# Optimization experiments

Measured on AMD Instinct MI355X. Metric: run time of the kernel, lower is better.

The kernel has to match this reference:

```python
import jax, jax.numpy as jnp
import numpy as np

NEG_SLOPE = 0.2

def _gat_layer(x, src, dst, W, a_s, a_d, b, concat):
    # x: [N, F_in], W: [F_in, H*C], a_s/a_d: [H, C]
    N = x.shape[0]
    H, C = a_s.shape
    h = (x @ W).reshape(N, H, C)                       # per-head projection
    al_s = jnp.sum(h * a_s, axis=-1)                   # [N, H]
    al_d = jnp.sum(h * a_d, axis=-1)                   # [N, H]
    e = jax.nn.leaky_relu(al_s[src] + al_d[dst], NEG_SLOPE)  # [E, H]
    # segment softmax over incoming edges of each dst node
    m = jax.ops.segment_max(e, dst, num_segments=N)    # [N, H]
    ex = jnp.exp(e - m[dst])
    denom = jax.ops.segment_sum(ex, dst, num_segments=N)
    alpha = ex / denom[dst]                            # [E, H]
    msg = h[src] * alpha[:, :, None]                   # [E, H, C]
    out = jax.ops.segment_sum(msg, dst, num_segments=N)  # [N, H, C]
    if concat:
        return out.reshape(N, H * C) + b
    return out.mean(axis=1) + b


def setup_inputs() -> dict:
    key = jax.random.key(0)
    ks = jax.random.split(key, 12)
    N, F_in, H, C1, LAT, E = 16384, 512, 4, 128, 64, 262144
    x = jax.random.normal(ks[0], (N, F_in), dtype=jnp.float32)
    edge_index = jax.random.randint(ks[1], (2, E), 0, N, dtype=jnp.int64)
    s = 0.05
    return {
        'x': x,
        'edge_index': edge_index,
        'W1': jax.random.normal(ks[2], (F_in, H * C1), dtype=jnp.float32) * s,
        'a_src1': jax.random.normal(ks[3], (H, C1), dtype=jnp.float32) * s,
        'a_dst1': jax.random.normal(ks[4], (H, C1), dtype=jnp.float32) * s,
        'b1': jax.random.normal(ks[5], (H * C1,), dtype=jnp.float32) * s,
        'W2': jax.random.normal(ks[6], (H * C1, H * LAT), dtype=jnp.float32) * s,
        'a_src2': jax.random.normal(ks[7], (H, LAT), dtype=jnp.float32) * s,
        'a_dst2': jax.random.normal(ks[8], (H, LAT), dtype=jnp.float32) * s,
        'b2': jax.random.normal(ks[9], (LAT,), dtype=jnp.float32) * s,
    }


def reference(x, edge_index, W1, a_src1, a_dst1, b1, W2, a_src2, a_dst2, b2):
    N = x.shape[0]
    # PyG GATConv default add_self_loops=True
    loop = jnp.arange(N, dtype=edge_index.dtype)
    src = jnp.concatenate([edge_index[0], loop])
    dst = jnp.concatenate([edge_index[1], loop])
    h = jax.nn.relu(_gat_layer(x, src, dst, W1, a_src1, a_dst1, b1, concat=True))
    out = _gat_layer(h, src, dst, W2, a_src2, a_dst2, b2, concat=False)
    return out
```

## Files before the change

kernel.cpp:

```cpp
#include <hip/hip_runtime.h>
#include <stdint.h>
#include <stddef.h>
#include <limits.h>

typedef __bf16 bf16;
typedef __bf16 bf16x4 __attribute__((ext_vector_type(4)));
typedef __bf16 bf16x8 __attribute__((ext_vector_type(8)));
typedef float  f32x4  __attribute__((ext_vector_type(4)));

static __device__ __forceinline__ float lrelu(float x) { return x > 0.f ? x : 0.2f * x; }
static __device__ __forceinline__ float san(float v) { return (fabsf(v) < 1e4f) ? v : 0.0f; }
static __device__ __forceinline__ float wexp(float e) { return __expf(fminf(e, 30.f)); }

static __device__ __forceinline__ void async_load16(const bf16* g, bf16* l) {
  __builtin_amdgcn_global_load_lds((const __attribute__((address_space(1))) void*)g,
                                   (__attribute__((address_space(3))) void*)l, 16, 0, 0);
}


__global__ __launch_bounds__(256) void prep_all(const float* __restrict__ x,
                                                bf16* __restrict__ xb,
                                                int* __restrict__ counts,
                                                const float* __restrict__ W1,
                                                const float* __restrict__ W2,
                                                bf16* __restrict__ W1T,
                                                bf16* __restrict__ W2T,
                                                int NX, int N) {
  int b = blockIdx.x;
  const int NCVT = NX >> 10;
  if (b < NCVT) {
    int i = b * 1024 + threadIdx.x * 4;
    f32x4 v = *(const f32x4*)(x + i);
    bf16x4 o;
#pragma unroll
    for (int k = 0; k < 4; ++k) o[k] = (bf16)san(v[k]);
    *(bf16x4*)(xb + i) = o;
    return;
  }
  b -= NCVT;
  if (b < N / 256) { counts[b * 256 + threadIdx.x] = 0; return; }
  b -= N / 256;
  __shared__ bf16 t[32][33];
  const float* in; bf16* out; int R, C, bx, by;
  if (b < 256) { in = W1; out = W1T; R = 512; C = 512; by = b >> 4; bx = b & 15; }
  else         { b -= 256; in = W2; out = W2T; R = 512; C = 256; by = b >> 3; bx = b & 7; }
  const int lane = threadIdx.x & 31, r8 = threadIdx.x >> 5;
#pragma unroll
  for (int k = 0; k < 4; ++k) {
    int r = by * 32 + r8 + k * 8, c = bx * 32 + lane;
    t[lane][r8 + k * 8] = (bf16)san(in[(size_t)r * C + c]);
  }
  __syncthreads();
#pragma unroll
  for (int k = 0; k < 4; ++k) {
    int oc = bx * 32 + r8 + k * 8;
    out[(size_t)oc * R + by * 32 + lane] = t[r8 + k * 8][lane];
  }
}


__global__ void count_edges(const int* __restrict__ dst, int E, int* __restrict__ counts) {
  int e = blockIdx.x * 256 + threadIdx.x;
  if (e < E) atomicAdd(&counts[dst[e]], 1);
}

__global__ __launch_bounds__(1024) void scan_block_sums(const int* __restrict__ counts,
                                                        int* __restrict__ bsums) {
  __shared__ int ws[16];
  const int tid = threadIdx.x, lane = tid & 63, w = tid >> 6;
  int v = counts[blockIdx.x * 1024 + tid];
  for (int off = 32; off; off >>= 1) v += __shfl_xor(v, off);
  if (lane == 0) ws[w] = v;
  __syncthreads();
  if (tid == 0) {
    int s = 0;
#pragma unroll
    for (int k = 0; k < 16; ++k) s += ws[k];
    bsums[blockIdx.x] = s;
  }
}

__global__ __launch_bounds__(1024) void scan_apply(const int* __restrict__ counts,
                                                   const int* __restrict__ bsums,
                                                   int* __restrict__ row_ptr,
                                                   int* __restrict__ cursor, int N, int nb) {
  __shared__ int wsum[16];
  __shared__ int bpre[2];
  const int tid = threadIdx.x, lane = tid & 63, w = tid >> 6;
  const int gi = blockIdx.x * 1024 + tid;
  if (tid == 0) {
    int pre = 0, tot = 0;
    for (int k = 0; k < nb; ++k) {
      if (k < (int)blockIdx.x) pre += bsums[k];
      tot += bsums[k];
    }
    bpre[0] = pre; bpre[1] = tot;
  }
  int v = counts[gi];
  int s = v;
  for (int off = 1; off < 64; off <<= 1) {
    int t = __shfl_up(s, off);
    if (lane >= off) s += t;
  }
  if (lane == 63) wsum[w] = s;
  __syncthreads();
  if (w == 0 && lane < 16) {
    int ws = wsum[lane];
    int t2 = ws;
    for (int off = 1; off < 16; off <<= 1) {
      int t = __shfl_up(t2, off);
      if (lane >= off) t2 += t;
    }
    wsum[lane] = t2 - ws;
  }
  __syncthreads();
  int excl = bpre[0] + wsum[w] + s - v;
  row_ptr[gi] = excl;
  cursor[gi]  = excl;
  if (gi == N - 1) row_ptr[N] = bpre[1];
}

__global__ void scatter_edges(const int* __restrict__ src, const int* __restrict__ dst, int E,
                              int* __restrict__ cursor, int* __restrict__ csr_src) {
  int e = blockIdx.x * 256 + threadIdx.x;
  if (e < E) {
    int pos = atomicAdd(&cursor[dst[e]], 1);
    csr_src[pos] = src[e];
  }
}

__global__ __launch_bounds__(256) void sort_rows_wave(const int* __restrict__ row_ptr,
                                                      int* __restrict__ csr, int N) {
  const int wid  = (blockIdx.x * 256 + threadIdx.x) >> 6;
  const int lane = threadIdx.x & 63;
  if (wid >= N) return;
  const int beg = row_ptr[wid], end = row_ptr[wid + 1];
  const int len = end - beg;
  if (len <= 1) return;
  if (len <= 64) {
    int v = (lane < len) ? csr[beg + lane] : INT_MAX;
#pragma unroll
    for (int k = 2; k <= 64; k <<= 1) {
#pragma unroll
      for (int j = k >> 1; j > 0; j >>= 1) {
        int p = __shfl_xor(v, j);
        bool take_min = (((lane & k) == 0) == ((lane & j) == 0));
        v = take_min ? min(v, p) : max(v, p);
      }
    }
    if (lane < len) csr[beg + lane] = v;
  } else if (lane == 0) {
    for (int i = beg + 1; i < end; ++i) {
      int v = csr[i];
      int j = i - 1;
      while (j >= beg && csr[j] > v) { csr[j + 1] = csr[j]; --j; }
      csr[j + 1] = v;
    }
  }
}


__global__ __launch_bounds__(256) void gemm_al_l1(const bf16* __restrict__ A,
                                                  const bf16* __restrict__ BT,
                                                  bf16* __restrict__ C,
                                                  const float* __restrict__ a_s,
                                                  const float* __restrict__ a_d,
                                                  float* __restrict__ al_s,
                                                  float* __restrict__ al_d,
                                                  int M, int N, int K) {
  __shared__ __align__(16) bf16 As[128 * 32];
  __shared__ __align__(16) bf16 Bs[128 * 32];
  __shared__ float alred[2][128][2];
  const int tid  = threadIdx.x;
  const int lane = tid & 63;
  const int wave = tid >> 6;
  const int m0 = blockIdx.x * 128;
  const int n0 = blockIdx.y * 128;
  const int wm = (wave >> 1) * 64;
  const int wn = (wave & 1) * 64;

  f32x4 acc[4][4] = {};

  const int id0 = tid, id1 = tid + 256;
  const bf16* a0p = A  + (size_t)(m0 + (id0 >> 2)) * K + (id0 & 3) * 8;
  const bf16* a1p = A  + (size_t)(m0 + (id1 >> 2)) * K + (id1 & 3) * 8;
  const bf16* b0p = BT + (size_t)(n0 + (id0 >> 2)) * K + (id0 & 3) * 8;
  const bf16* b1p = BT + (size_t)(n0 + (id1 >> 2)) * K + (id1 & 3) * 8;

  const int kq = (lane >> 4) * 8;
  const int rA = wm + (lane & 15);
  const int rB = wn + (lane & 15);

  for (int k0 = 0; k0 < K; k0 += 32) {
    __syncthreads();
    async_load16(a0p + k0, &As[id0 * 8]);
    async_load16(a1p + k0, &As[id1 * 8]);
    async_load16(b0p + k0, &Bs[id0 * 8]);
    async_load16(b1p + k0, &Bs[id1 * 8]);
    __syncthreads();
    bf16x8 af[4], bfv[4];
#pragma unroll
    for (int i = 0; i < 4; ++i) af[i]  = *(const bf16x8*)&As[(rA + i * 16) * 32 + kq];
#pragma unroll
    for (int j = 0; j < 4; ++j) bfv[j] = *(const bf16x8*)&Bs[(rB + j * 16) * 32 + kq];
#pragma unroll
    for (int i = 0; i < 4; ++i)
#pragma unroll
      for (int j = 0; j < 4; ++j)
        acc[i][j] = __builtin_amdgcn_mfma_f32_16x16x32_bf16(af[i], bfv[j], acc[i][j], 0, 0, 0);
  }

  const int cc = lane & 15;
  const int rb = (lane >> 4) * 4;
#pragma unroll
  for (int i = 0; i < 4; ++i)
#pragma unroll
    for (int j = 0; j < 4; ++j) {
      int gcol = n0 + wn + j * 16 + cc;
#pragma unroll
      for (int r = 0; r < 4; ++r) {
        int grow = m0 + wm + i * 16 + rb + r;
        C[(size_t)grow * N + gcol] = (bf16)acc[i][j][r];
      }
    }

  {
    const int head = blockIdx.y;
    float asv[4], adv[4];
#pragma unroll
    for (int j = 0; j < 4; ++j) {
      int col = head * 128 + wn + j * 16 + cc;
      asv[j] = san(a_s[col]);
      adv[j] = san(a_d[col]);
    }
    const int wnh = wn >> 6;
#pragma unroll
    for (int i = 0; i < 4; ++i)
#pragma unroll
      for (int r = 0; r < 4; ++r) {
        float ps = 0.f, pd = 0.f;
#pragma unroll
        for (int j = 0; j < 4; ++j) { ps += acc[i][j][r] * asv[j]; pd += acc[i][j][r] * adv[j]; }
#pragma unroll
        for (int off = 1; off <= 8; off <<= 1) {
          ps += __shfl_xor(ps, off);
          pd += __shfl_xor(pd, off);
        }
        if (cc == 0) {
          int row = wm + i * 16 + rb + r;
          alred[wnh][row][0] = ps;
          alred[wnh][row][1] = pd;
        }
      }
    __syncthreads();
    if (tid < 128) {
      al_s[(size_t)(m0 + tid) * 4 + head] = alred[0][tid][0] + alred[1][tid][0];
      al_d[(size_t)(m0 + tid) * 4 + head] = alred[0][tid][1] + alred[1][tid][1];
    }
  }
}


__global__ __launch_bounds__(256) void gemm_al_l2(const bf16* __restrict__ A,
                                                  const bf16* __restrict__ BT,
                                                  bf16* __restrict__ C,
                                                  const float* __restrict__ a_s,
                                                  const float* __restrict__ a_d,
                                                  float* __restrict__ al_s,
                                                  float* __restrict__ al_d,
                                                  int M, int N, int K) {
  __shared__ __align__(16) bf16 As[64 * 32];
  __shared__ __align__(16) bf16 Bs[128 * 32];
  const int tid  = threadIdx.x;
  const int lane = tid & 63;
  const int wave = tid >> 6;
  const int m0 = blockIdx.x * 64;
  const int n0 = blockIdx.y * 128;
  const int wm = (wave >> 1) * 32;
  const int wn = (wave & 1) * 64;

  f32x4 acc[2][4] = {};

  const int tb = tid + 256;
  const bf16* ap  = A  + (size_t)(m0 + (tid >> 2)) * K + (tid & 3) * 8;
  const bf16* bp0 = BT + (size_t)(n0 + (tid >> 2)) * K + (tid & 3) * 8;
  const bf16* bp1 = BT + (size_t)(n0 + (tb  >> 2)) * K + (tb  & 3) * 8;

  const int kq = (lane >> 4) * 8;
  const int rA = wm + (lane & 15);
  const int rB = wn + (lane & 15);

  for (int k0 = 0; k0 < K; k0 += 32) {
    __syncthreads();
    async_load16(ap  + k0, &As[tid * 8]);
    async_load16(bp0 + k0, &Bs[tid * 8]);
    async_load16(bp1 + k0, &Bs[tb  * 8]);
    __syncthreads();
    bf16x8 af[2], bfv[4];
#pragma unroll
    for (int i = 0; i < 2; ++i) af[i]  = *(const bf16x8*)&As[(rA + i * 16) * 32 + kq];
#pragma unroll
    for (int j = 0; j < 4; ++j) bfv[j] = *(const bf16x8*)&Bs[(rB + j * 16) * 32 + kq];
#pragma unroll
    for (int i = 0; i < 2; ++i)
#pragma unroll
      for (int j = 0; j < 4; ++j)
        acc[i][j] = __builtin_amdgcn_mfma_f32_16x16x32_bf16(af[i], bfv[j], acc[i][j], 0, 0, 0);
  }

  const int cc = lane & 15;
  const int rb = (lane >> 4) * 4;
#pragma unroll
  for (int i = 0; i < 2; ++i)
#pragma unroll
    for (int j = 0; j < 4; ++j) {
      int gcol = n0 + wn + j * 16 + cc;
#pragma unroll
      for (int r = 0; r < 4; ++r) {
        int grow = m0 + wm + i * 16 + rb + r;
        C[(size_t)grow * N + gcol] = (bf16)acc[i][j][r];
      }
    }

  {
    const int head = blockIdx.y * 2 + (wn >> 6);
    float asv[4], adv[4];
#pragma unroll
    for (int j = 0; j < 4; ++j) {
      int col = head * 64 + j * 16 + cc;
      asv[j] = san(a_s[col]);
      adv[j] = san(a_d[col]);
    }
#pragma unroll
    for (int i = 0; i < 2; ++i)
#pragma unroll
      for (int r = 0; r < 4; ++r) {
        float ps = 0.f, pd = 0.f;
#pragma unroll
        for (int j = 0; j < 4; ++j) { ps += acc[i][j][r] * asv[j]; pd += acc[i][j][r] * adv[j]; }
#pragma unroll
        for (int off = 1; off <= 8; off <<= 1) {
          ps += __shfl_xor(ps, off);
          pd += __shfl_xor(pd, off);
        }
        if (cc == 0) {
          int row = m0 + wm + i * 16 + rb + r;
          al_s[(size_t)row * 4 + head] = ps;
          al_d[(size_t)row * 4 + head] = pd;
        }
      }
  }
}


__global__ __launch_bounds__(64) void aggregate1_f(const bf16* __restrict__ h1,
                                                   const float* __restrict__ al_s,
                                                   const float* __restrict__ al_d,
                                                   const int* __restrict__ row_ptr,
                                                   const int* __restrict__ csr_src,
                                                   const float* __restrict__ bias,
                                                   bf16* __restrict__ out) {
  __shared__ int   sIdx[64];
  __shared__ f32x4 sW[64];
  const int n = blockIdx.x, lane = threadIdx.x;
  const int cb = lane * 8;
  const int hd = lane >> 4;
  const int beg = row_ptr[n], end = row_ptr[n + 1];
  const f32x4 alsn = *(const f32x4*)(al_s + (size_t)n * 4);
  const f32x4 aldn = *(const f32x4*)(al_d + (size_t)n * 4);

  const float wself = wexp(lrelu(alsn[hd] + aldn[hd]));
  bf16x8 hv0 = *(const bf16x8*)(h1 + (size_t)n * 512 + cb);
  float acc[8];
#pragma unroll
  for (int k = 0; k < 8; ++k) acc[k] = wself * (float)hv0[k];

  f32x4 Lv = {0.f, 0.f, 0.f, 0.f};
  if (lane == 0) {
#pragma unroll
    for (int h = 0; h < 4; ++h) Lv[h] = wexp(lrelu(alsn[h] + aldn[h]));
  }
  for (int c0 = beg; c0 < end; c0 += 64) {
    const int cl = min(64, end - c0);
    __syncthreads();
    if (lane < cl) {
      int s = csr_src[c0 + lane];
      sIdx[lane] = s;
      f32x4 a = *(const f32x4*)(al_s + (size_t)s * 4);
      f32x4 w;
#pragma unroll
      for (int h = 0; h < 4; ++h) w[h] = wexp(lrelu(a[h] + aldn[h]));
      sW[lane] = w;
#pragma unroll
      for (int h = 0; h < 4; ++h) Lv[h] += w[h];
    }
    __syncthreads();
#pragma unroll 4
    for (int j = 0; j < cl; ++j) {
      int s = sIdx[j];
      float a = sW[j][hd];
      bf16x8 hv = *(const bf16x8*)(h1 + (size_t)s * 512 + cb);
#pragma unroll
      for (int k = 0; k < 8; ++k) acc[k] += a * (float)hv[k];
    }
  }
  for (int off = 32; off; off >>= 1) {
#pragma unroll
    for (int h = 0; h < 4; ++h) Lv[h] += __shfl_xor(Lv[h], off);
  }
  const float inv = 1.0f / Lv[hd];
  bf16x8 ov;
#pragma unroll
  for (int k = 0; k < 8; ++k)
    ov[k] = (bf16)fmaxf(acc[k] * inv + san(bias[cb + k]), 0.f);
  *(bf16x8*)(out + (size_t)n * 512 + cb) = ov;
}


__global__ __launch_bounds__(64) void aggregate2_f(const bf16* __restrict__ h2,
                                                   const float* __restrict__ al_s,
                                                   const float* __restrict__ al_d,
                                                   const int* __restrict__ row_ptr,
                                                   const int* __restrict__ csr_src,
                                                   const float* __restrict__ bias,
                                                   float* __restrict__ out) {
  __shared__ int   sIdx[64];
  __shared__ f32x4 sW[64];
  const int n = blockIdx.x, lane = threadIdx.x;
  const int hd = lane >> 4;
  const int cb = lane * 4;
  const int beg = row_ptr[n], end = row_ptr[n + 1];
  const f32x4 alsn = *(const f32x4*)(al_s + (size_t)n * 4);
  const f32x4 aldn = *(const f32x4*)(al_d + (size_t)n * 4);

  const float wself = wexp(lrelu(alsn[hd] + aldn[hd]));
  bf16x4 hv0 = *(const bf16x4*)(h2 + (size_t)n * 256 + cb);
  float acc0 = wself * (float)hv0[0], acc1 = wself * (float)hv0[1];
  float acc2 = wself * (float)hv0[2], acc3 = wself * (float)hv0[3];
  f32x4 Lv = {0.f, 0.f, 0.f, 0.f};
  if (lane == 0) {
#pragma unroll
    for (int h = 0; h < 4; ++h) Lv[h] = wexp(lrelu(alsn[h] + aldn[h]));
  }
  for (int c0 = beg; c0 < end; c0 += 64) {
    const int cl = min(64, end - c0);
    __syncthreads();
    if (lane < cl) {
      int s = csr_src[c0 + lane];
      sIdx[lane] = s;
      f32x4 a = *(const f32x4*)(al_s + (size_t)s * 4);
      f32x4 w;
#pragma unroll
      for (int h = 0; h < 4; ++h) w[h] = wexp(lrelu(a[h] + aldn[h]));
      sW[lane] = w;
#pragma unroll
      for (int h = 0; h < 4; ++h) Lv[h] += w[h];
    }
    __syncthreads();
#pragma unroll 4
    for (int j = 0; j < cl; ++j) {
      int s = sIdx[j];
      float a = sW[j][hd];
      bf16x4 hv = *(const bf16x4*)(h2 + (size_t)s * 256 + cb);
      acc0 += a * (float)hv[0];
      acc1 += a * (float)hv[1];
      acc2 += a * (float)hv[2];
      acc3 += a * (float)hv[3];
    }
  }
  for (int off = 32; off; off >>= 1) {
#pragma unroll
    for (int h = 0; h < 4; ++h) Lv[h] += __shfl_xor(Lv[h], off);
  }
  const float inv = 1.0f / Lv[hd];
  acc0 *= inv; acc1 *= inv; acc2 *= inv; acc3 *= inv;
  acc0 += __shfl_xor(acc0, 16); acc1 += __shfl_xor(acc1, 16);
  acc2 += __shfl_xor(acc2, 16); acc3 += __shfl_xor(acc3, 16);
  acc0 += __shfl_xor(acc0, 32); acc1 += __shfl_xor(acc1, 32);
  acc2 += __shfl_xor(acc2, 32); acc3 += __shfl_xor(acc3, 32);
  if (lane < 16) {
    int ob = lane * 4;
    f32x4 ov;
    ov[0] = 0.25f * acc0 + san(bias[ob]);
    ov[1] = 0.25f * acc1 + san(bias[ob + 1]);
    ov[2] = 0.25f * acc2 + san(bias[ob + 2]);
    ov[3] = 0.25f * acc3 + san(bias[ob + 3]);
    *(f32x4*)(out + (size_t)n * 64 + ob) = ov;
  }
}


extern "C" void kernel_launch(void* const* d_in, const int* in_sizes, int n_in,
                              void* d_out, int out_size, void* d_ws, size_t ws_size,
                              hipStream_t stream) {
  const float* x   = (const float*)d_in[0];
  const int*   ei  = (const int*)d_in[1];
  const float* W1  = (const float*)d_in[2];
  const float* as1 = (const float*)d_in[3];
  const float* ad1 = (const float*)d_in[4];
  const float* b1  = (const float*)d_in[5];
  const float* W2  = (const float*)d_in[6];
  const float* as2 = (const float*)d_in[7];
  const float* ad2 = (const float*)d_in[8];
  const float* b2  = (const float*)d_in[9];
  float* outp = (float*)d_out;

  const int N = in_sizes[0] / 512;
  const int E = in_sizes[1] / 2;
  const int* src = ei;
  const int* dst = ei + E;

  char* p = (char*)d_ws;
  auto alloc = [&](size_t bytes) {
    char* r = p;
    p += (bytes + 255) & ~(size_t)255;
    return r;
  };
  bf16* xb    = (bf16*)alloc((size_t)N * 512 * 2);
  bf16* h1    = (bf16*)alloc((size_t)N * 512 * 2);
  bf16* hbuf  = (bf16*)alloc((size_t)N * 512 * 2);
  bf16* W1T   = (bf16*)alloc((size_t)512 * 512 * 2);
  bf16* W2T   = (bf16*)alloc((size_t)256 * 512 * 2);
  float* al_s1 = (float*)alloc((size_t)N * 4 * 4);
  float* al_d1 = (float*)alloc((size_t)N * 4 * 4);
  float* al_s2 = (float*)alloc((size_t)N * 4 * 4);
  float* al_d2 = (float*)alloc((size_t)N * 4 * 4);
  int* counts  = (int*)alloc((size_t)N * 4);
  int* row_ptr = (int*)alloc((size_t)(N + 1) * 4);
  int* cursor  = (int*)alloc((size_t)N * 4);
  int* csr_src = (int*)alloc((size_t)E * 4);
  int* bsums   = (int*)alloc((size_t)32 * 4);
  bf16* h2 = h1;

  const int nb = N / 1024;
  const int NX = N * 512;

  prep_all<<<(NX >> 10) + N / 256 + 256 + 128, 256, 0, stream>>>(
      x, xb, counts, W1, W2, W1T, W2T, NX, N);

  count_edges<<<(E + 255) / 256, 256, 0, stream>>>(dst, E, counts);
  scan_block_sums<<<nb, 1024, 0, stream>>>(counts, bsums);
  scan_apply<<<nb, 1024, 0, stream>>>(counts, bsums, row_ptr, cursor, N, nb);
  scatter_edges<<<(E + 255) / 256, 256, 0, stream>>>(src, dst, E, cursor, csr_src);
  sort_rows_wave<<<(N * 64 + 255) / 256, 256, 0, stream>>>(row_ptr, csr_src, N);

  gemm_al_l1<<<dim3(N / 128, 4), 256, 0, stream>>>(xb, W1T, h1, as1, ad1, al_s1, al_d1,
                                                   N, 512, 512);
  aggregate1_f<<<N, 64, 0, stream>>>(h1, al_s1, al_d1, row_ptr, csr_src, b1, hbuf);

  gemm_al_l2<<<dim3(N / 64, 2), 256, 0, stream>>>(hbuf, W2T, h2, as2, ad2, al_s2, al_d2,
                                                  N, 256, 512);
  aggregate2_f<<<N, 64, 0, stream>>>(h2, al_s2, al_d2, row_ptr, csr_src, b2, outp);
}
```

Baseline: 223.5 us.

## Merge graph preprocessing kernels into one cooperative kernel with grid syncs

Replaces six separate preprocessing launches (convert/transpose, edge count, two-stage scan, scatter, row sort) with a single cooperative kernel of 512 blocks that uses grid-wide barriers between phases. The scan is restructured into 64 blocks of 256, plus a single-wave scan of block sums. This removes per-launch overhead and inter-kernel gaps. In exchange it adds grid.sync costs and limits parallelism in the grid-stride phases to 512 blocks.

```diff
diff --git a/kernel.cpp b/kernel.cpp
--- a/kernel.cpp
+++ b/kernel.cpp
@@ -1,7 +1,10 @@
 #include <hip/hip_runtime.h>
+#include <hip/hip_cooperative_groups.h>
 #include <stdint.h>
 #include <stddef.h>
 #include <limits.h>
+
+namespace cg = cooperative_groups;
 
 typedef __bf16 bf16;
 typedef __bf16 bf16x4 __attribute__((ext_vector_type(4)));
@@ -18,143 +21,130 @@
 }
 
 
-__global__ __launch_bounds__(256) void prep_all(const float* __restrict__ x,
-                                                bf16* __restrict__ xb,
-                                                int* __restrict__ counts,
-                                                const float* __restrict__ W1,
-                                                const float* __restrict__ W2,
-                                                bf16* __restrict__ W1T,
-                                                bf16* __restrict__ W2T,
-                                                int NX, int N) {
-  int b = blockIdx.x;
-  const int NCVT = NX >> 10;
-  if (b < NCVT) {
-    int i = b * 1024 + threadIdx.x * 4;
-    f32x4 v = *(const f32x4*)(x + i);
+__global__ __launch_bounds__(256) void coop_build(const float* __restrict__ x,
+                                                  bf16* __restrict__ xb,
+                                                  const float* __restrict__ W1,
+                                                  const float* __restrict__ W2,
+                                                  bf16* __restrict__ W1T,
+                                                  bf16* __restrict__ W2T,
+                                                  const int* __restrict__ src,
+                                                  const int* __restrict__ dst,
+                                                  int E,
+                                                  int* __restrict__ counts,
+                                                  int* __restrict__ row_ptr,
+                                                  int* __restrict__ cursor,
+                                                  int* __restrict__ bsums,
+                                                  int* __restrict__ csr_src,
+                                                  int N, int NX) {
+  cg::grid_group grid = cg::this_grid();
+  __shared__ bf16 t[32][33];
+  __shared__ int  ws[4];
+  const int tid  = threadIdx.x;
+  const int gsz  = gridDim.x * 256;
+  const int gid  = blockIdx.x * 256 + tid;
+  const int lane = tid & 63;
+  const int wv   = tid >> 6;
+
+  for (int i = gid; i < N; i += gsz) counts[i] = 0;
+  for (int i = gid; i < (NX >> 2); i += gsz) {
+    f32x4 v = *(const f32x4*)(x + (size_t)i * 4);
     bf16x4 o;
 #pragma unroll
     for (int k = 0; k < 4; ++k) o[k] = (bf16)san(v[k]);
-    *(bf16x4*)(xb + i) = o;
-    return;
-  }
-  b -= NCVT;
-  if (b < N / 256) { counts[b * 256 + threadIdx.x] = 0; return; }
-  b -= N / 256;
-  __shared__ bf16 t[32][33];
-  const float* in; bf16* out; int R, C, bx, by;
-  if (b < 256) { in = W1; out = W1T; R = 512; C = 512; by = b >> 4; bx = b & 15; }
-  else         { b -= 256; in = W2; out = W2T; R = 512; C = 256; by = b >> 3; bx = b & 7; }
-  const int lane = threadIdx.x & 31, r8 = threadIdx.x >> 5;
-#pragma unroll
-  for (int k = 0; k < 4; ++k) {
-    int r = by * 32 + r8 + k * 8, c = bx * 32 + lane;
-    t[lane][r8 + k * 8] = (bf16)san(in[(size_t)r * C + c]);
-  }
-  __syncthreads();
-#pragma unroll
-  for (int k = 0; k < 4; ++k) {
-    int oc = bx * 32 + r8 + k * 8;
-    out[(size_t)oc * R + by * 32 + lane] = t[r8 + k * 8][lane];
-  }
-}
-
-
-__global__ void count_edges(const int* __restrict__ dst, int E, int* __restrict__ counts) {
-  int e = blockIdx.x * 256 + threadIdx.x;
-  if (e < E) atomicAdd(&counts[dst[e]], 1);
-}
-
-__global__ __launch_bounds__(1024) void scan_block_sums(const int* __restrict__ counts,
-                                                        int* __restrict__ bsums) {
-  __shared__ int ws[16];
-  const int tid = threadIdx.x, lane = tid & 63, w = tid >> 6;
-  int v = counts[blockIdx.x * 1024 + tid];
-  for (int off = 32; off; off >>= 1) v += __shfl_xor(v, off);
-  if (lane == 0) ws[w] = v;
-  __syncthreads();
-  if (tid == 0) {
-    int s = 0;
-#pragma unroll
-    for (int k = 0; k < 16; ++k) s += ws[k];
-    bsums[blockIdx.x] = s;
-  }
-}
-
-__global__ __launch_bounds__(1024) void scan_apply(const int* __restrict__ counts,
-                                                   const int* __restrict__ bsums,
-                                                   int* __restrict__ row_ptr,
-                                                   int* __restrict__ cursor, int N, int nb) {
-  __shared__ int wsum[16];
-  __shared__ int bpre[2];
-  const int tid = threadIdx.x, lane = tid & 63, w = tid >> 6;
-  const int gi = blockIdx.x * 1024 + tid;
-  if (tid == 0) {
-    int pre = 0, tot = 0;
-    for (int k = 0; k < nb; ++k) {
-      if (k < (int)blockIdx.x) pre += bsums[k];
-      tot += bsums[k];
-    }
-    bpre[0] = pre; bpre[1] = tot;
-  }
-  int v = counts[gi];
-  int s = v;
-  for (int off = 1; off < 64; off <<= 1) {
-    int t = __shfl_up(s, off);
-    if (lane >= off) s += t;
-  }
-  if (lane == 63) wsum[w] = s;
-  __syncthreads();
-  if (w == 0 && lane < 16) {
-    int ws = wsum[lane];
-    int t2 = ws;
-    for (int off = 1; off < 16; off <<= 1) {
-      int t = __shfl_up(t2, off);
-      if (lane >= off) t2 += t;
-    }
-    wsum[lane] = t2 - ws;
-  }
-  __syncthreads();
-  int excl = bpre[0] + wsum[w] + s - v;
-  row_ptr[gi] = excl;
-  cursor[gi]  = excl;
-  if (gi == N - 1) row_ptr[N] = bpre[1];
-}
-
-__global__ void scatter_edges(const int* __restrict__ src, const int* __restrict__ dst, int E,
-                              int* __restrict__ cursor, int* __restrict__ csr_src) {
-  int e = blockIdx.x * 256 + threadIdx.x;
-  if (e < E) {
+    *(bf16x4*)(xb + (size_t)i * 4) = o;
+  }
+  for (int b = blockIdx.x; b < 384; b += gridDim.x) {
+    const float* in; bf16* out; int R, C, bx, by, bb = b;
+    if (bb < 256) { in = W1; out = W1T; R = 512; C = 512; by = bb >> 4; bx = bb & 15; }
+    else          { bb -= 256; in = W2; out = W2T; R = 512; C = 256; by = bb >> 3; bx = bb & 7; }
+    const int l32 = tid & 31, r8 = tid >> 5;
+    __syncthreads();
+#pragma unroll
+    for (int k = 0; k < 4; ++k) {
+      int r = by * 32 + r8 + k * 8, c = bx * 32 + l32;
+      t[l32][r8 + k * 8] = (bf16)san(in[(size_t)r * C + c]);
+    }
+    __syncthreads();
+#pragma unroll
+    for (int k = 0; k < 4; ++k) {
+      int oc = bx * 32 + r8 + k * 8;
+      out[(size_t)oc * R + by * 32 + l32] = t[r8 + k * 8][l32];
+    }
+  }
+  grid.sync();
+
+  for (int e = gid; e < E; e += gsz) atomicAdd(&counts[dst[e]], 1);
+  grid.sync();
+
+  if (blockIdx.x < 64) {
+    const int c  = blockIdx.x;
+    const int gi = c * 256 + tid;
+    int v = counts[gi];
+    int s = v;
+    for (int off = 1; off < 64; off <<= 1) {
+      int u = __shfl_up(s, off);
+      if (lane >= off) s += u;
+    }
+    if (lane == 63) ws[wv] = s;
+    __syncthreads();
+    int wpre = 0;
+#pragma unroll
+    for (int k = 0; k < 4; ++k) if (k < wv) wpre += ws[k];
+    row_ptr[gi] = wpre + s - v;
+    if (tid == 255) bsums[c] = wpre + s;
+  }
+  grid.sync();
+
+  if (blockIdx.x == 0 && tid < 64) {
+    int v = bsums[tid];
+    int s = v;
+    for (int off = 1; off < 64; off <<= 1) {
+      int u = __shfl_up(s, off);
+      if (tid >= off) s += u;
+    }
+    bsums[tid] = s - v;
+    if (tid == 63) row_ptr[N] = s;
+  }
+  grid.sync();
+
+  if (blockIdx.x < 64) {
+    const int gi = blockIdx.x * 256 + tid;
+    int rp = row_ptr[gi] + bsums[blockIdx.x];
+    row_ptr[gi] = rp;
+    cursor[gi]  = rp;
+  }
+  grid.sync();
+
+  for (int e = gid; e < E; e += gsz) {
     int pos = atomicAdd(&cursor[dst[e]], 1);
     csr_src[pos] = src[e];
   }
-}
-
-__global__ __launch_bounds__(256) void sort_rows_wave(const int* __restrict__ row_ptr,
-                                                      int* __restrict__ csr, int N) {
-  const int wid  = (blockIdx.x * 256 + threadIdx.x) >> 6;
-  const int lane = threadIdx.x & 63;
-  if (wid >= N) return;
-  const int beg = row_ptr[wid], end = row_ptr[wid + 1];
-  const int len = end - beg;
-  if (len <= 1) return;
-  if (len <= 64) {
-    int v = (lane < len) ? csr[beg + lane] : INT_MAX;
-#pragma unroll
-    for (int k = 2; k <= 64; k <<= 1) {
-#pragma unroll
-      for (int j = k >> 1; j > 0; j >>= 1) {
-        int p = __shfl_xor(v, j);
-        bool take_min = (((lane & k) == 0) == ((lane & j) == 0));
-        v = take_min ? min(v, p) : max(v, p);
+  grid.sync();
+
+  const int nwaves = gsz >> 6;
+  for (int n = (gid >> 6); n < N; n += nwaves) {
+    const int beg = row_ptr[n], end = row_ptr[n + 1];
+    const int len = end - beg;
+    if (len <= 1) continue;
+    if (len <= 64) {
+      int v = (lane < len) ? csr_src[beg + lane] : INT_MAX;
+#pragma unroll
+      for (int k = 2; k <= 64; k <<= 1) {
+#pragma unroll
+        for (int j = k >> 1; j > 0; j >>= 1) {
+          int p = __shfl_xor(v, j);
+          bool take_min = (((lane & k) == 0) == ((lane & j) == 0));
+          v = take_min ? min(v, p) : max(v, p);
+        }
       }
-    }
-    if (lane < len) csr[beg + lane] = v;
-  } else if (lane == 0) {
-    for (int i = beg + 1; i < end; ++i) {
-      int v = csr[i];
-      int j = i - 1;
-      while (j >= beg && csr[j] > v) { csr[j + 1] = csr[j]; --j; }
-      csr[j + 1] = v;
+      if (lane < len) csr_src[beg + lane] = v;
+    } else if (lane == 0) {
+      for (int i = beg + 1; i < end; ++i) {
+        int v = csr_src[i];
+        int j = i - 1;
+        while (j >= beg && csr_src[j] > v) { csr_src[j + 1] = csr_src[j]; --j; }
+        csr_src[j + 1] = v;
+      }
     }
   }
 }
@@ -505,8 +495,8 @@
   const float* b2  = (const float*)d_in[9];
   float* outp = (float*)d_out;
 
-  const int N = in_sizes[0] / 512;
-  const int E = in_sizes[1] / 2;
+  int N = in_sizes[0] / 512;
+  int E = in_sizes[1] / 2;
   const int* src = ei;
   const int* dst = ei + E;
 
@@ -529,20 +519,17 @@
   int* row_ptr = (int*)alloc((size_t)(N + 1) * 4);
   int* cursor  = (int*)alloc((size_t)N * 4);
   int* csr_src = (int*)alloc((size_t)E * 4);
-  int* bsums   = (int*)alloc((size_t)32 * 4);
+  int* bsums   = (int*)alloc((size_t)128 * 4);
   bf16* h2 = h1;
 
-  const int nb = N / 1024;
-  const int NX = N * 512;
-
-  prep_all<<<(NX >> 10) + N / 256 + 256 + 128, 256, 0, stream>>>(
-      x, xb, counts, W1, W2, W1T, W2T, NX, N);
-
-  count_edges<<<(E + 255) / 256, 256, 0, stream>>>(dst, E, counts);
-  scan_block_sums<<<nb, 1024, 0, stream>>>(counts, bsums);
-  scan_apply<<<nb, 1024, 0, stream>>>(counts, bsums, row_ptr, cursor, N, nb);
-  scatter_edges<<<(E + 255) / 256, 256, 0, stream>>>(src, dst, E, cursor, csr_src);
-  sort_rows_wave<<<(N * 64 + 255) / 256, 256, 0, stream>>>(row_ptr, csr_src, N);
+  int NX = N * 512;
+
+  {
+    void* args[] = {(void*)&x, (void*)&xb, (void*)&W1, (void*)&W2, (void*)&W1T, (void*)&W2T,
+                    (void*)&src, (void*)&dst, (void*)&E, (void*)&counts, (void*)&row_ptr,
+                    (void*)&cursor, (void*)&bsums, (void*)&csr_src, (void*)&N, (void*)&NX};
+    hipLaunchCooperativeKernel((void*)coop_build, dim3(512), dim3(256), args, 0, stream);
+  }
 
   gemm_al_l1<<<dim3(N / 128, 4), 256, 0, stream>>>(xb, W1T, h1, as1, ad1, al_s1, al_d1,
                                                    N, 512, 512);
```

Result: slower. 583.6 us (+161.2%).

## Fuse row sorting into layer-1 aggregation and merge scan kernels

Applied to the files above, without the earlier changes.

Removes the separate per-row CSR sort kernel and does the sort inside aggregate1 instead: a wave bitonic sort for short rows, whose sorted values are used directly and written back for layer 2, and a serial insertion sort on lane 0 for long rows. The two-pass block-sum scan becomes a single kernel in which each block recomputes its prefix by summing all earlier counts. Barriers in the single-wave aggregation loops are dropped, relying on the 64-thread block being one wave. This saves two kernel launches and one pass over csr_src. In exchange, the prefix computation is redundant and grows with block index, and correctness depends on wave-synchronous shared-memory behaviour.

```diff
diff --git a/kernel.cpp b/kernel.cpp
--- a/kernel.cpp
+++ b/kernel.cpp
@@ -64,38 +64,22 @@
   if (e < E) atomicAdd(&counts[dst[e]], 1);
 }
 
-__global__ __launch_bounds__(1024) void scan_block_sums(const int* __restrict__ counts,
-                                                        int* __restrict__ bsums) {
-  __shared__ int ws[16];
+__global__ __launch_bounds__(1024) void scan_all(const int* __restrict__ counts,
+                                                 int* __restrict__ row_ptr,
+                                                 int* __restrict__ cursor, int N) {
+  __shared__ int redbuf[16];
+  __shared__ int wsum[16];
   const int tid = threadIdx.x, lane = tid & 63, w = tid >> 6;
-  int v = counts[blockIdx.x * 1024 + tid];
-  for (int off = 32; off; off >>= 1) v += __shfl_xor(v, off);
-  if (lane == 0) ws[w] = v;
+  const int b = blockIdx.x;
+  const int gi = b * 1024 + tid;
+  int pre = 0;
+  for (int i = tid; i < b * 1024; i += 1024) pre += counts[i];
+  for (int off = 32; off; off >>= 1) pre += __shfl_xor(pre, off);
+  if (lane == 0) redbuf[w] = pre;
   __syncthreads();
-  if (tid == 0) {
-    int s = 0;
-#pragma unroll
-    for (int k = 0; k < 16; ++k) s += ws[k];
-    bsums[blockIdx.x] = s;
-  }
-}
-
-__global__ __launch_bounds__(1024) void scan_apply(const int* __restrict__ counts,
-                                                   const int* __restrict__ bsums,
-                                                   int* __restrict__ row_ptr,
-                                                   int* __restrict__ cursor, int N, int nb) {
-  __shared__ int wsum[16];
-  __shared__ int bpre[2];
-  const int tid = threadIdx.x, lane = tid & 63, w = tid >> 6;
-  const int gi = blockIdx.x * 1024 + tid;
-  if (tid == 0) {
-    int pre = 0, tot = 0;
-    for (int k = 0; k < nb; ++k) {
-      if (k < (int)blockIdx.x) pre += bsums[k];
-      tot += bsums[k];
-    }
-    bpre[0] = pre; bpre[1] = tot;
-  }
+  int bpre = 0;
+#pragma unroll
+  for (int k = 0; k < 16; ++k) bpre += redbuf[k];
   int v = counts[gi];
   int s = v;
   for (int off = 1; off < 64; off <<= 1) {
@@ -114,10 +98,10 @@
     wsum[lane] = t2 - ws;
   }
   __syncthreads();
-  int excl = bpre[0] + wsum[w] + s - v;
+  int excl = bpre + wsum[w] + s - v;
   row_ptr[gi] = excl;
   cursor[gi]  = excl;
-  if (gi == N - 1) row_ptr[N] = bpre[1];
+  if (gi == N - 1) row_ptr[N] = excl + v;
 }
 
 __global__ void scatter_edges(const int* __restrict__ src, const int* __restrict__ dst, int E,
@@ -126,36 +110,6 @@
   if (e < E) {
     int pos = atomicAdd(&cursor[dst[e]], 1);
     csr_src[pos] = src[e];
-  }
-}
-
-__global__ __launch_bounds__(256) void sort_rows_wave(const int* __restrict__ row_ptr,
-                                                      int* __restrict__ csr, int N) {
-  const int wid  = (blockIdx.x * 256 + threadIdx.x) >> 6;
-  const int lane = threadIdx.x & 63;
-  if (wid >= N) return;
-  const int beg = row_ptr[wid], end = row_ptr[wid + 1];
-  const int len = end - beg;
-  if (len <= 1) return;
-  if (len <= 64) {
-    int v = (lane < len) ? csr[beg + lane] : INT_MAX;
-#pragma unroll
-    for (int k = 2; k <= 64; k <<= 1) {
-#pragma unroll
-      for (int j = k >> 1; j > 0; j >>= 1) {
-        int p = __shfl_xor(v, j);
-        bool take_min = (((lane & k) == 0) == ((lane & j) == 0));
-        v = take_min ? min(v, p) : max(v, p);
-      }
-    }
-    if (lane < len) csr[beg + lane] = v;
-  } else if (lane == 0) {
-    for (int i = beg + 1; i < end; ++i) {
-      int v = csr[i];
-      int j = i - 1;
-      while (j >= beg && csr[j] > v) { csr[j + 1] = csr[j]; --j; }
-      csr[j + 1] = v;
-    }
   }
 }
 
@@ -357,7 +311,7 @@
                                                    const float* __restrict__ al_s,
                                                    const float* __restrict__ al_d,
                                                    const int* __restrict__ row_ptr,
-                                                   const int* __restrict__ csr_src,
+                                                   int* __restrict__ csr_src,
                                                    const float* __restrict__ bias,
                                                    bf16* __restrict__ out) {
   __shared__ int   sIdx[64];
@@ -366,6 +320,7 @@
   const int cb = lane * 8;
   const int hd = lane >> 4;
   const int beg = row_ptr[n], end = row_ptr[n + 1];
+  const int len = end - beg;
   const f32x4 alsn = *(const f32x4*)(al_s + (size_t)n * 4);
   const f32x4 aldn = *(const f32x4*)(al_d + (size_t)n * 4);
 
@@ -380,13 +335,24 @@
 #pragma unroll
     for (int h = 0; h < 4; ++h) Lv[h] = wexp(lrelu(alsn[h] + aldn[h]));
   }
-  for (int c0 = beg; c0 < end; c0 += 64) {
-    const int cl = min(64, end - c0);
-    __syncthreads();
-    if (lane < cl) {
-      int s = csr_src[c0 + lane];
-      sIdx[lane] = s;
-      f32x4 a = *(const f32x4*)(al_s + (size_t)s * 4);
+
+  if (len <= 64) {
+    int v = (lane < len) ? csr_src[beg + lane] : INT_MAX;
+    if (len > 1) {
+#pragma unroll
+      for (int k = 2; k <= 64; k <<= 1) {
+#pragma unroll
+        for (int j = k >> 1; j > 0; j >>= 1) {
+          int p = __shfl_xor(v, j);
+          bool take_min = (((lane & k) == 0) == ((lane & j) == 0));
+          v = take_min ? min(v, p) : max(v, p);
+        }
+      }
+      if (lane < len) csr_src[beg + lane] = v;
+    }
+    if (lane < len) {
+      sIdx[lane] = v;
+      f32x4 a = *(const f32x4*)(al_s + (size_t)v * 4);
       f32x4 w;
 #pragma unroll
       for (int h = 0; h < 4; ++h) w[h] = wexp(lrelu(a[h] + aldn[h]));
@@ -394,16 +360,48 @@
 #pragma unroll
       for (int h = 0; h < 4; ++h) Lv[h] += w[h];
     }
-    __syncthreads();
 #pragma unroll 4
-    for (int j = 0; j < cl; ++j) {
+    for (int j = 0; j < len; ++j) {
       int s = sIdx[j];
       float a = sW[j][hd];
       bf16x8 hv = *(const bf16x8*)(h1 + (size_t)s * 512 + cb);
 #pragma unroll
       for (int k = 0; k < 8; ++k) acc[k] += a * (float)hv[k];
     }
-  }
+  } else {
+    if (lane == 0) {
+      for (int i = beg + 1; i < end; ++i) {
+        int v = csr_src[i];
+        int j = i - 1;
+        while (j >= beg && csr_src[j] > v) { csr_src[j + 1] = csr_src[j]; --j; }
+        csr_src[j + 1] = v;
+      }
+    }
+    __syncthreads();
+    for (int c0 = beg; c0 < end; c0 += 64) {
+      const int cl = min(64, end - c0);
+      if (lane < cl) {
+        int s = csr_src[c0 + lane];
+        sIdx[lane] = s;
+        f32x4 a = *(const f32x4*)(al_s + (size_t)s * 4);
+        f32x4 w;
+#pragma unroll
+        for (int h = 0; h < 4; ++h) w[h] = wexp(lrelu(a[h] + aldn[h]));
+        sW[lane] = w;
+#pragma unroll
+        for (int h = 0; h < 4; ++h) Lv[h] += w[h];
+      }
+#pragma unroll 4
+      for (int j = 0; j < cl; ++j) {
+        int s = sIdx[j];
+        float a = sW[j][hd];
+        bf16x8 hv = *(const bf16x8*)(h1 + (size_t)s * 512 + cb);
+#pragma unroll
+        for (int k = 0; k < 8; ++k) acc[k] += a * (float)hv[k];
+      }
+    }
+  }
+
   for (int off = 32; off; off >>= 1) {
 #pragma unroll
     for (int h = 0; h < 4; ++h) Lv[h] += __shfl_xor(Lv[h], off);
@@ -444,7 +442,6 @@
   }
   for (int c0 = beg; c0 < end; c0 += 64) {
     const int cl = min(64, end - c0);
-    __syncthreads();
     if (lane < cl) {
       int s = csr_src[c0 + lane];
       sIdx[lane] = s;
@@ -456,7 +453,6 @@
 #pragma unroll
       for (int h = 0; h < 4; ++h) Lv[h] += w[h];
     }
-    __syncthreads();
 #pragma unroll 4
     for (int j = 0; j < cl; ++j) {
       int s = sIdx[j];
@@ -529,20 +525,16 @@
   int* row_ptr = (int*)alloc((size_t)(N + 1) * 4);
   int* cursor  = (int*)alloc((size_t)N * 4);
   int* csr_src = (int*)alloc((size_t)E * 4);
-  int* bsums   = (int*)alloc((size_t)32 * 4);
   bf16* h2 = h1;
 
-  const int nb = N / 1024;
   const int NX = N * 512;
 
   prep_all<<<(NX >> 10) + N / 256 + 256 + 128, 256, 0, stream>>>(
       x, xb, counts, W1, W2, W1T, W2T, NX, N);
 
   count_edges<<<(E + 255) / 256, 256, 0, stream>>>(dst, E, counts);
-  scan_block_sums<<<nb, 1024, 0, stream>>>(counts, bsums);
-  scan_apply<<<nb, 1024, 0, stream>>>(counts, bsums, row_ptr, cursor, N, nb);
+  scan_all<<<N / 1024, 1024, 0, stream>>>(counts, row_ptr, cursor, N);
   scatter_edges<<<(E + 255) / 256, 256, 0, stream>>>(src, dst, E, cursor, csr_src);
-  sort_rows_wave<<<(N * 64 + 255) / 256, 256, 0, stream>>>(row_ptr, csr_src, N);
 
   gemm_al_l1<<<dim3(N / 128, 4), 256, 0, stream>>>(xb, W1T, h1, as1, ad1, al_s1, al_d1,
                                                    N, 512, 512);
```

Measured after the change: 217.3 us. 1.03x faster.
